# Performance work log

Hardware: AMD Instinct MI355X
Metric: run time of the kernel (lower is better)

The kernel has to match this reference:

```python
import jax, jax.numpy as jnp
import numpy as np

B, H, N, K, D = 8, 8, 4096, 32, 16  # batch, heads, points, neighbors, head depth
K_OUT = H * D


def setup_inputs() -> dict:
    key = jax.random.key(0)
    ks = jax.random.split(key, 8)
    return {
        "q": jax.random.normal(ks[0], (B, H, N, 1, D), dtype=jnp.float32),
        "k": jax.random.normal(ks[1], (B, H, N, D, K), dtype=jnp.float32),
        "v": jax.random.normal(ks[2], (B, H, N, K, D), dtype=jnp.float32),
        "xyz": jax.random.normal(ks[3], (B, N, K, 3), dtype=jnp.float32),
        "W1": jax.random.normal(ks[4], (3, H), dtype=jnp.float32) * 0.5,
        "b1": jax.random.normal(ks[5], (H,), dtype=jnp.float32) * 0.1,
        "W2": jax.random.normal(ks[6], (3, K_OUT), dtype=jnp.float32) * 0.5,
        "b2": jax.random.normal(ks[7], (K_OUT,), dtype=jnp.float32) * 0.1,
    }


def reference(q, k, v, xyz, W1, b1, W2, b2):
    # energy_xyz: Linear(3->H) on xyz [B,N,K,3] -> [B,N,K,H] -> [B,H,N,1,K]
    e_xyz = jnp.einsum("bnkc,ch->bhnk", xyz, W1) + b1[None, :, None, None]
    e_xyz = e_xyz[:, :, :, None, :]                      # [B,H,N,1,K]
    energy = jnp.matmul(q, k) + e_xyz                    # [B,H,N,1,K]
    scale = jnp.float32(np.sqrt(D))
    attn = jax.nn.softmax(energy / scale, axis=-1)       # [B,H,N,1,K]
    # v_xyz: Linear(3->H*D) then raw reshape [B,N,K,H*D] -> [B,H,N,K,D]
    v_xyz = jnp.einsum("bnkc,co->bnko", xyz, W2) + b2    # [B,N,K,H*D]
    v_xyz = v_xyz.reshape(B, H, N, K, D)                 # memory reshape, as torch .view
    v = v + v_xyz
    x = jnp.matmul(attn, v)[:, :, :, 0, :]               # [B,H,N,D]
    return jnp.transpose(x, (0, 2, 1, 3))                # [B,N,H,D]
```

## Files before the change

### kernel.cpp

```cpp
#include <hip/hip_runtime.h>

#define B_ 8
#define H_ 8
#define N_ 4096
#define K_ 32
#define D_ 16

__device__ __forceinline__ float4 ld4(const float* p) {
    return *reinterpret_cast<const float4*>(p);
}

__global__ __launch_bounds__(256) void pe_attn_kernel(
    const float* __restrict__ q, const float* __restrict__ kmat,
    const float* __restrict__ vmat, const float* __restrict__ xyz,
    const float* __restrict__ W1, const float* __restrict__ b1,
    const float* __restrict__ W2, const float* __restrict__ b2,
    float* __restrict__ out)
{
    const int lane = threadIdx.x & 63;
    const int wid  = threadIdx.x >> 6;
    const int row  = (blockIdx.x << 2) + wid;
    const int n  = row & (N_ - 1);
    const int bh = row >> 12;
    const int h  = bh & (H_ - 1);
    const int b  = bh >> 3;

    __shared__ float attn_s[4][32];

    const size_t row512 = (size_t)row * (D_ * K_);
    const float* krow = kmat + row512;
    const float* vrow = vmat + row512;
    const float* qrow = q + (size_t)row * D_;

    const int dg = lane >> 3;
    const int kg = lane & 7;
    const int kq = lane >> 2;
    const int d0 = (lane & 3) << 2;

    float4 k1 = ld4(krow + 4 * lane);
    float4 k2 = ld4(krow + 256 + 4 * lane);
    float4 v1 = ld4(vrow + 4 * lane);
    float4 v2 = ld4(vrow + 256 + 4 * lane);

    float qa = qrow[dg] * 0.25f;
    float qb = qrow[8 + dg] * 0.25f;

    const float* xrow = xyz + (size_t)(b * N_ + n) * (K_ * 3) + 12 * kg;
    float4 f0 = ld4(xrow);
    float4 f1 = ld4(xrow + 4);
    float4 f2 = ld4(xrow + 8);
    float w10 = W1[h] * 0.25f, w11 = W1[H_ + h] * 0.25f, w12 = W1[2 * H_ + h] * 0.25f;
    float bb1 = b1[h] * 0.25f;

    const int nsrc = (h << 9) | (n >> 3);
    const int kb   = (n & 7) << 2;
    const int ks1  = kb + (kq >> 3);
    const int ks2  = kb + 2 + (kq >> 3);
    const int o1   = ((kq & 7) << 4) | d0;

    const float* xvb = xyz + (size_t)(b * N_ + nsrc) * (K_ * 3);
    float X1 = xvb[ks1 * 3], Y1 = xvb[ks1 * 3 + 1], Z1 = xvb[ks1 * 3 + 2];
    float X2 = xvb[ks2 * 3], Y2 = xvb[ks2 * 3 + 1], Z2 = xvb[ks2 * 3 + 2];
    float4 w20 = ld4(W2 + o1);
    float4 w21 = ld4(W2 + 128 + o1);
    float4 w22 = ld4(W2 + 256 + o1);
    float4 bb2 = ld4(b2 + o1);

    float4 e;
    e.x = fmaf(qa, k1.x, qb * k2.x);
    e.y = fmaf(qa, k1.y, qb * k2.y);
    e.z = fmaf(qa, k1.z, qb * k2.z);
    e.w = fmaf(qa, k1.w, qb * k2.w);

    #pragma unroll
    for (int m = 8; m <= 32; m <<= 1) {
        e.x += __shfl_xor(e.x, m);
        e.y += __shfl_xor(e.y, m);
        e.z += __shfl_xor(e.z, m);
        e.w += __shfl_xor(e.w, m);
    }

    e.x += fmaf(f0.x, w10, fmaf(f0.y, w11, fmaf(f0.z, w12, bb1)));
    e.y += fmaf(f0.w, w10, fmaf(f1.x, w11, fmaf(f1.y, w12, bb1)));
    e.z += fmaf(f1.z, w10, fmaf(f1.w, w11, fmaf(f2.x, w12, bb1)));
    e.w += fmaf(f2.y, w10, fmaf(f2.z, w11, fmaf(f2.w, w12, bb1)));

    float mx = fmaxf(fmaxf(e.x, e.y), fmaxf(e.z, e.w));
    #pragma unroll
    for (int m = 1; m <= 4; m <<= 1) mx = fmaxf(mx, __shfl_xor(mx, m));

    float4 p;
    p.x = __expf(e.x - mx);
    p.y = __expf(e.y - mx);
    p.z = __expf(e.z - mx);
    p.w = __expf(e.w - mx);
    float s = (p.x + p.y) + (p.z + p.w);
    #pragma unroll
    for (int m = 1; m <= 4; m <<= 1) s += __shfl_xor(s, m);
    float invs = 1.0f / s;

    if (lane < 8) {
        float4 a4 = make_float4(p.x * invs, p.y * invs, p.z * invs, p.w * invs);
        *reinterpret_cast<float4*>(&attn_s[wid][4 * kg]) = a4;
    }
    __builtin_amdgcn_wave_barrier();
    float a1 = attn_s[wid][kq];
    float a2 = attn_s[wid][16 + kq];
    __builtin_amdgcn_wave_barrier();

    float4 acc;
    {
        float vx;
        vx = fmaf(X1, w20.x, fmaf(Y1, w21.x, fmaf(Z1, w22.x, bb2.x)));
        acc.x = a1 * (v1.x + vx);
        vx = fmaf(X1, w20.y, fmaf(Y1, w21.y, fmaf(Z1, w22.y, bb2.y)));
        acc.y = a1 * (v1.y + vx);
        vx = fmaf(X1, w20.z, fmaf(Y1, w21.z, fmaf(Z1, w22.z, bb2.z)));
        acc.z = a1 * (v1.z + vx);
        vx = fmaf(X1, w20.w, fmaf(Y1, w21.w, fmaf(Z1, w22.w, bb2.w)));
        acc.w = a1 * (v1.w + vx);

        vx = fmaf(X2, w20.x, fmaf(Y2, w21.x, fmaf(Z2, w22.x, bb2.x)));
        acc.x = fmaf(a2, v2.x + vx, acc.x);
        vx = fmaf(X2, w20.y, fmaf(Y2, w21.y, fmaf(Z2, w22.y, bb2.y)));
        acc.y = fmaf(a2, v2.y + vx, acc.y);
        vx = fmaf(X2, w20.z, fmaf(Y2, w21.z, fmaf(Z2, w22.z, bb2.z)));
        acc.z = fmaf(a2, v2.z + vx, acc.z);
        vx = fmaf(X2, w20.w, fmaf(Y2, w21.w, fmaf(Z2, w22.w, bb2.w)));
        acc.w = fmaf(a2, v2.w + vx, acc.w);
    }

    #pragma unroll
    for (int m = 4; m <= 32; m <<= 1) {
        acc.x += __shfl_xor(acc.x, m);
        acc.y += __shfl_xor(acc.y, m);
        acc.z += __shfl_xor(acc.z, m);
        acc.w += __shfl_xor(acc.w, m);
    }

    if (lane < 4) {
        float* op = out + ((size_t)(b * N_ + n) * H_ + h) * D_ + d0;
        *reinterpret_cast<float4*>(op) = acc;
    }
}

extern "C" void kernel_launch(void* const* d_in, const int* in_sizes, int n_in,
                              void* d_out, int out_size, void* d_ws, size_t ws_size,
                              hipStream_t stream) {
    const float* q   = (const float*)d_in[0];
    const float* k   = (const float*)d_in[1];
    const float* v   = (const float*)d_in[2];
    const float* xyz = (const float*)d_in[3];
    const float* W1  = (const float*)d_in[4];
    const float* b1  = (const float*)d_in[5];
    const float* W2  = (const float*)d_in[6];
    const float* b2  = (const float*)d_in[7];
    float* out = (float*)d_out;

    dim3 grid(B_ * H_ * N_ / 4);
    dim3 block(256);
    hipLaunchKernelGGL(pe_attn_kernel, grid, block, 0, stream,
                       q, k, v, xyz, W1, b1, W2, b2, out);
}
```

Baseline: 1.015 ms.

## Process 16 rows per wave with double-buffered register prefetch

Each wave now handles 16 consecutive rows instead of one, and the grid shrinks from 65536 to 4096 blocks. The next row's k, v, q and xyz loads are issued into a second register set while the current row is computed. Per-head constants (W1, b1, W2, b2) are loaded once per wave rather than once per row. This trades more registers and fewer resident blocks for better memory-latency hiding and lower per-block launch overhead.

After: 1.004 ms. About the same (-1.0%).

```diff
diff --git a/kernel.cpp b/kernel.cpp
--- a/kernel.cpp
+++ b/kernel.cpp
@@ -5,10 +5,18 @@
 #define N_ 4096
 #define K_ 32
 #define D_ 16
+#define ROWS_ 16
+#define NBLK_ 4096
 
 __device__ __forceinline__ float4 ld4(const float* p) {
     return *reinterpret_cast<const float4*>(p);
 }
+
+struct RowRegs {
+    float4 k1, k2, v1, v2;
+    float4 f0, f1, f2;
+    float qa, qb;
+};
 
 __global__ __launch_bounds__(256) void pe_attn_kernel(
     const float* __restrict__ q, const float* __restrict__ kmat,
@@ -19,128 +27,140 @@
 {
     const int lane = threadIdx.x & 63;
     const int wid  = threadIdx.x >> 6;
-    const int row  = (blockIdx.x << 2) + wid;
-    const int n  = row & (N_ - 1);
-    const int bh = row >> 12;
+
+    const int bh = blockIdx.x & 63;
     const int h  = bh & (H_ - 1);
     const int b  = bh >> 3;
-
-    __shared__ float attn_s[4][32];
-
-    const size_t row512 = (size_t)row * (D_ * K_);
-    const float* krow = kmat + row512;
-    const float* vrow = vmat + row512;
-    const float* qrow = q + (size_t)row * D_;
+    const int n0 = (((blockIdx.x >> 6) << 2) | wid) << 4;
 
     const int dg = lane >> 3;
     const int kg = lane & 7;
     const int kq = lane >> 2;
     const int d0 = (lane & 3) << 2;
+    const int khi = kq >> 3;
 
-    float4 k1 = ld4(krow + 4 * lane);
-    float4 k2 = ld4(krow + 256 + 4 * lane);
-    float4 v1 = ld4(vrow + 4 * lane);
-    float4 v2 = ld4(vrow + 256 + 4 * lane);
+    __shared__ float attn_s[4][2][32];
 
-    float qa = qrow[dg] * 0.25f;
-    float qb = qrow[8 + dg] * 0.25f;
+    const float w10 = W1[h] * 0.25f, w11 = W1[H_ + h] * 0.25f, w12 = W1[2 * H_ + h] * 0.25f;
+    const float bb1 = b1[h] * 0.25f;
+    const int o1 = ((kq & 7) << 4) | d0;
+    const float4 w20 = ld4(W2 + o1);
+    const float4 w21 = ld4(W2 + 128 + o1);
+    const float4 w22 = ld4(W2 + 256 + o1);
+    const float4 bb2 = ld4(b2 + o1);
 
-    const float* xrow = xyz + (size_t)(b * N_ + n) * (K_ * 3) + 12 * kg;
-    float4 f0 = ld4(xrow);
-    float4 f1 = ld4(xrow + 4);
-    float4 f2 = ld4(xrow + 8);
-    float w10 = W1[h] * 0.25f, w11 = W1[H_ + h] * 0.25f, w12 = W1[2 * H_ + h] * 0.25f;
-    float bb1 = b1[h] * 0.25f;
+    const size_t rowbase = (size_t)bh * N_ + n0;
+    const float* kp = kmat + rowbase * (D_ * K_);
+    const float* vp = vmat + rowbase * (D_ * K_);
+    const float* qp = q + rowbase * D_;
+    const float* xp = xyz + (size_t)(b * N_ + n0) * (K_ * 3) + 12 * kg;
+    const float* xvb = xyz + (size_t)b * N_ * (K_ * 3);
+    float* op = out + ((size_t)(b * N_ + n0) * H_ + h) * D_ + d0;
 
-    const int nsrc = (h << 9) | (n >> 3);
-    const int kb   = (n & 7) << 2;
-    const int ks1  = kb + (kq >> 3);
-    const int ks2  = kb + 2 + (kq >> 3);
-    const int o1   = ((kq & 7) << 4) | d0;
+    auto pref = [&](const float* kr, const float* vr, const float* qr,
+                    const float* xr) {
+        RowRegs r;
+        r.k1 = ld4(kr + 4 * lane);
+        r.k2 = ld4(kr + 256 + 4 * lane);
+        r.v1 = ld4(vr + 4 * lane);
+        r.v2 = ld4(vr + 256 + 4 * lane);
+        r.qa = qr[dg];
+        r.qb = qr[8 + dg];
+        r.f0 = ld4(xr);
+        r.f1 = ld4(xr + 4);
+        r.f2 = ld4(xr + 8);
+        return r;
+    };
 
-    const float* xvb = xyz + (size_t)(b * N_ + nsrc) * (K_ * 3);
-    float X1 = xvb[ks1 * 3], Y1 = xvb[ks1 * 3 + 1], Z1 = xvb[ks1 * 3 + 2];
-    float X2 = xvb[ks2 * 3], Y2 = xvb[ks2 * 3 + 1], Z2 = xvb[ks2 * 3 + 2];
-    float4 w20 = ld4(W2 + o1);
-    float4 w21 = ld4(W2 + 128 + o1);
-    float4 w22 = ld4(W2 + 256 + o1);
-    float4 bb2 = ld4(b2 + o1);
+    auto compute = [&](const RowRegs& r, int n, float* asrow, float* opn) {
+        const int nsrc = (h << 9) | (n >> 3);
+        const int ks1 = ((n & 7) << 2) + khi;
+        const float* xv = xvb + (size_t)nsrc * (K_ * 3) + ks1 * 3;
+        const float X1 = xv[0], Y1 = xv[1], Z1 = xv[2];
+        const float X2 = xv[6], Y2 = xv[7], Z2 = xv[8];
 
-    float4 e;
-    e.x = fmaf(qa, k1.x, qb * k2.x);
-    e.y = fmaf(qa, k1.y, qb * k2.y);
-    e.z = fmaf(qa, k1.z, qb * k2.z);
-    e.w = fmaf(qa, k1.w, qb * k2.w);
+        const float qa = r.qa * 0.25f;
+        const float qb = r.qb * 0.25f;
 
-    #pragma unroll
-    for (int m = 8; m <= 32; m <<= 1) {
-        e.x += __shfl_xor(e.x, m);
-        e.y += __shfl_xor(e.y, m);
-        e.z += __shfl_xor(e.z, m);
-        e.w += __shfl_xor(e.w, m);
-    }
+        float4 e;
+        e.x = fmaf(qa, r.k1.x, qb * r.k2.x);
+        e.y = fmaf(qa, r.k1.y, qb * r.k2.y);
+        e.z = fmaf(qa, r.k1.z, qb * r.k2.z);
+        e.w = fmaf(qa, r.k1.w, qb * r.k2.w);
+        #pragma unroll
+        for (int m = 8; m <= 32; m <<= 1) {
+            e.x += __shfl_xor(e.x, m);
+            e.y += __shfl_xor(e.y, m);
+            e.z += __shfl_xor(e.z, m);
+            e.w += __shfl_xor(e.w, m);
+        }
+        e.x += fmaf(r.f0.x, w10, fmaf(r.f0.y, w11, fmaf(r.f0.z, w12, bb1)));
+        e.y += fmaf(r.f0.w, w10, fmaf(r.f1.x, w11, fmaf(r.f1.y, w12, bb1)));
+        e.z += fmaf(r.f1.z, w10, fmaf(r.f1.w, w11, fmaf(r.f2.x, w12, bb1)));
+        e.w += fmaf(r.f2.y, w10, fmaf(r.f2.z, w11, fmaf(r.f2.w, w12, bb1)));
 
-    e.x += fmaf(f0.x, w10, fmaf(f0.y, w11, fmaf(f0.z, w12, bb1)));
-    e.y += fmaf(f0.w, w10, fmaf(f1.x, w11, fmaf(f1.y, w12, bb1)));
-    e.z += fmaf(f1.z, w10, fmaf(f1.w, w11, fmaf(f2.x, w12, bb1)));
-    e.w += fmaf(f2.y, w10, fmaf(f2.z, w11, fmaf(f2.w, w12, bb1)));
+        float mx = fmaxf(fmaxf(e.x, e.y), fmaxf(e.z, e.w));
+        #pragma unroll
+        for (int m = 1; m <= 4; m <<= 1) mx = fmaxf(mx, __shfl_xor(mx, m));
 
-    float mx = fmaxf(fmaxf(e.x, e.y), fmaxf(e.z, e.w));
-    #pragma unroll
-    for (int m = 1; m <= 4; m <<= 1) mx = fmaxf(mx, __shfl_xor(mx, m));
+        float4 p;
+        p.x = __expf(e.x - mx);
+        p.y = __expf(e.y - mx);
+        p.z = __expf(e.z - mx);
+        p.w = __expf(e.w - mx);
+        float s = (p.x + p.y) + (p.z + p.w);
+        #pragma unroll
+        for (int m = 1; m <= 4; m <<= 1) s += __shfl_xor(s, m);
+        float invs = 1.0f / s;
 
-    float4 p;
-    p.x = __expf(e.x - mx);
-    p.y = __expf(e.y - mx);
-    p.z = __expf(e.z - mx);
-    p.w = __expf(e.w - mx);
-    float s = (p.x + p.y) + (p.z + p.w);
-    #pragma unroll
-    for (int m = 1; m <= 4; m <<= 1) s += __shfl_xor(s, m);
-    float invs = 1.0f / s;
+        if (lane < 8) {
+            float4 a4 = make_float4(p.x * invs, p.y * invs, p.z * invs, p.w * invs);
+            *reinterpret_cast<float4*>(asrow + 4 * kg) = a4;
+        }
+        __builtin_amdgcn_wave_barrier();
+        float a1 = asrow[kq];
+        float a2 = asrow[16 + kq];
+        __builtin_amdgcn_wave_barrier();
 
-    if (lane < 8) {
-        float4 a4 = make_float4(p.x * invs, p.y * invs, p.z * invs, p.w * invs);
-        *reinterpret_cast<float4*>(&attn_s[wid][4 * kg]) = a4;
-    }
-    __builtin_amdgcn_wave_barrier();
-    float a1 = attn_s[wid][kq];
-    float a2 = attn_s[wid][16 + kq];
-    __builtin_amdgcn_wave_barrier();
-
-    float4 acc;
-    {
+        float4 acc;
         float vx;
         vx = fmaf(X1, w20.x, fmaf(Y1, w21.x, fmaf(Z1, w22.x, bb2.x)));
-        acc.x = a1 * (v1.x + vx);
+        acc.x = a1 * (r.v1.x + vx);
         vx = fmaf(X1, w20.y, fmaf(Y1, w21.y, fmaf(Z1, w22.y, bb2.y)));
-        acc.y = a1 * (v1.y + vx);
+        acc.y = a1 * (r.v1.y + vx);
         vx = fmaf(X1, w20.z, fmaf(Y1, w21.z, fmaf(Z1, w22.z, bb2.z)));
-        acc.z = a1 * (v1.z + vx);
+        acc.z = a1 * (r.v1.z + vx);
         vx = fmaf(X1, w20.w, fmaf(Y1, w21.w, fmaf(Z1, w22.w, bb2.w)));
-        acc.w = a1 * (v1.w + vx);
+        acc.w = a1 * (r.v1.w + vx);
 
         vx = fmaf(X2, w20.x, fmaf(Y2, w21.x, fmaf(Z2, w22.x, bb2.x)));
-        acc.x = fmaf(a2, v2.x + vx, acc.x);
+        acc.x = fmaf(a2, r.v2.x + vx, acc.x);
         vx = fmaf(X2, w20.y, fmaf(Y2, w21.y, fmaf(Z2, w22.y, bb2.y)));
-        acc.y = fmaf(a2, v2.y + vx, acc.y);
+        acc.y = fmaf(a2, r.v2.y + vx, acc.y);
         vx = fmaf(X2, w20.z, fmaf(Y2, w21.z, fmaf(Z2, w22.z, bb2.z)));
-        acc.z = fmaf(a2, v2.z + vx, acc.z);
+        acc.z = fmaf(a2, r.v2.z + vx, acc.z);
         vx = fmaf(X2, w20.w, fmaf(Y2, w21.w, fmaf(Z2, w22.w, bb2.w)));
-        acc.w = fmaf(a2, v2.w + vx, acc.w);
-    }
+        acc.w = fmaf(a2, r.v2.w + vx, acc.w);
 
-    #pragma unroll
-    for (int m = 4; m <= 32; m <<= 1) {
-        acc.x += __shfl_xor(acc.x, m);
-        acc.y += __shfl_xor(acc.y, m);
-        acc.z += __shfl_xor(acc.z, m);
-        acc.w += __shfl_xor(acc.w, m);
-    }
+        #pragma unroll
+        for (int m = 4; m <= 32; m <<= 1) {
+            acc.x += __shfl_xor(acc.x, m);
+            acc.y += __shfl_xor(acc.y, m);
+            acc.z += __shfl_xor(acc.z, m);
+            acc.w += __shfl_xor(acc.w, m);
+        }
+        if (lane < 4) *reinterpret_cast<float4*>(opn) = acc;
+    };
 
-    if (lane < 4) {
-        float* op = out + ((size_t)(b * N_ + n) * H_ + h) * D_ + d0;
-        *reinterpret_cast<float4*>(op) = acc;
+    RowRegs A = pref(kp, vp, qp, xp);
+    #pragma unroll 1
+    for (int i = 0; i < ROWS_; i += 2) {
+        RowRegs Bv = pref(kp + 512, vp + 512, qp + 16, xp + 96);
+        compute(A, n0 + i, &attn_s[wid][0][0], op);
+        if (i + 2 < ROWS_)
+            A = pref(kp + 1024, vp + 1024, qp + 32, xp + 192);
+        compute(Bv, n0 + i + 1, &attn_s[wid][1][0], op + 128);
+        kp += 1024; vp += 1024; qp += 32; xp += 192; op += 256;
     }
 }
 
@@ -157,7 +177,7 @@
     const float* b2  = (const float*)d_in[7];
     float* out = (float*)d_out;
 
-    dim3 grid(B_ * H_ * N_ / 4);
+    dim3 grid(NBLK_);
     dim3 block(256);
     hipLaunchKernelGGL(pe_attn_kernel, grid, block, 0, stream,
                        q, k, v, xyz, W1, b1, W2, b2, out);
```
